# Optimization experiments

Measured on AMD Instinct MI355X. Metric: run time of the kernel, lower is better.

The kernel has to match this reference:

```python
import jax, jax.numpy as jnp
import numpy as np

N_NODES = 100000


def gcn_conv(x, W, b, src, dst, n):
    """PyG GCNConv: add self-loops, symmetric degree norm, linear, scatter-add."""
    loop = jnp.arange(n, dtype=src.dtype)
    s = jnp.concatenate([src, loop])  # source nodes (message origin)
    d = jnp.concatenate([dst, loop])  # target nodes (aggregation)
    deg = jax.ops.segment_sum(jnp.ones_like(d, dtype=x.dtype), d, num_segments=n)
    dinv = jnp.where(deg > 0, jax.lax.rsqrt(deg), 0.0)
    norm = dinv[s] * dinv[d]  # [E+N]
    h = x @ W  # [N, out]
    msg = h[s] * norm[:, None]  # [E+N, out]
    return jax.ops.segment_sum(msg, d, num_segments=n) + b


def setup_inputs() -> dict:
    key = jax.random.key(0)
    ks = jax.random.split(key, 8)
    n, e, din, dh, dout = N_NODES, 3200000, 128, 64, 6
    x = jax.random.normal(ks[0], (n, din), dtype=jnp.float32)
    edge_index = jax.random.randint(ks[1], (2, e), 0, n, dtype=jnp.int64)
    sc = lambda f: 1.0 / np.sqrt(f)
    W1 = jax.random.normal(ks[2], (din, dh), dtype=jnp.float32) * sc(din)
    b1 = jnp.zeros((dh,), dtype=jnp.float32)
    W2 = jax.random.normal(ks[3], (dh, dh), dtype=jnp.float32) * sc(dh)
    b2 = jnp.zeros((dh,), dtype=jnp.float32)
    W3 = jax.random.normal(ks[4], (dh, dout), dtype=jnp.float32) * sc(dh)
    b3 = jnp.zeros((dout,), dtype=jnp.float32)
    return {"x": x, "edge_index": edge_index, "W1": W1, "b1": b1,
            "W2": W2, "b2": b2, "W3": W3, "b3": b3}


def reference(x, edge_index, W1, b1, W2, b2, W3, b3):
    n = x.shape[0]
    src, dst = edge_index[0], edge_index[1]
    # eval mode: dropout is identity
    h = jax.nn.relu(gcn_conv(x, W1, b1, src, dst, n))
    h = jax.nn.relu(gcn_conv(h, W2, b2, src, dst, n))
    h = gcn_conv(h, W3, b3, src, dst, n)
    return jax.nn.log_softmax(h, axis=1)
```

## Files before the change

kernel.cpp:

```cpp
#include <hip/hip_runtime.h>
#include <hip/hip_fp16.h>
#include <math.h>


#define WS_ALIGN(x) (((x) + 255) & ~(size_t)255)
#define BKN 128
#define CAP 4608
#define EPT 8
#define BIN_THR 512
#define BIN_CHUNK (BIN_THR * EPT)

typedef _Float16 half8 __attribute__((ext_vector_type(8)));
typedef float floatx4 __attribute__((ext_vector_type(4)));

__global__ __launch_bounds__(BIN_THR) void bin_kernel(
    const int* __restrict__ src, const int* __restrict__ dst,
    int* __restrict__ cur, int* __restrict__ slab, int E, int NB) {
    __shared__ int counts[784];
    const int tid = threadIdx.x;
    const int base = blockIdx.x * BIN_CHUNK + tid * EPT;
    for (int i = tid; i < NB; i += BIN_THR) counts[i] = 0;
    __syncthreads();
    int b[EPT], w[EPT], lpos[EPT];
    #pragma unroll
    for (int k = 0; k < EPT; ++k) {
        int e = base + k;
        if (e < E) {
            int s = src[e], d = dst[e];
            b[k] = d >> 7;
            w[k] = (s << 7) | (d & 127);
        } else b[k] = -1;
    }
    #pragma unroll
    for (int k = 0; k < EPT; ++k)
        if (b[k] >= 0) lpos[k] = atomicAdd(&counts[b[k]], 1);
    __syncthreads();
    for (int i = tid; i < NB; i += BIN_THR) {
        int c = counts[i];
        counts[i] = c ? atomicAdd(&cur[i], c) : 0;
    }
    __syncthreads();
    #pragma unroll
    for (int k = 0; k < EPT; ++k) {
        if (b[k] >= 0) {
            int pos = counts[b[k]] + lpos[k];
            if (pos < CAP) slab[(size_t)b[k] * CAP + pos] = w[k];
        }
    }
}

__global__ __launch_bounds__(512) void bucket_sort_kernel(
    const int* __restrict__ slab, const int* __restrict__ cur,
    int* __restrict__ srcS, int2* __restrict__ rows,
    float* __restrict__ dinv, int n) {
    __shared__ int cnt[BKN], s[BKN], cursor[BKN];
    const int b = blockIdx.x, tid = threadIdx.x;
    const int m = min(cur[b], CAP);
    const int* sp = slab + (size_t)b * CAP;
    if (tid < BKN) cnt[tid] = 0;
    __syncthreads();
    for (int j = tid; j < m; j += 512) atomicAdd(&cnt[sp[j] & (BKN - 1)], 1);
    __syncthreads();
    if (tid < BKN) s[tid] = cnt[tid];
    __syncthreads();
    for (int off = 1; off < BKN; off <<= 1) {
        int v = 0;
        if (tid < BKN && tid >= off) v = s[tid - off];
        __syncthreads();
        if (tid < BKN) s[tid] += v;
        __syncthreads();
    }
    if (tid < BKN) {
        int ofs = s[tid] - cnt[tid];
        cursor[tid] = ofs;
        int node = b * BKN + tid;
        if (node < n) {
            rows[node] = make_int2(b * CAP + ofs, b * CAP + ofs + cnt[tid]);
            dinv[node] = rsqrtf((float)(cnt[tid] + 1));
        }
    }
    __syncthreads();
    for (int j = tid; j < m; j += 512) {
        int w = sp[j];
        int p = atomicAdd(&cursor[w & (BKN - 1)], 1);
        srcS[(size_t)b * CAP + p] = w >> 7;
    }
}

template <int K>
__global__ __launch_bounds__(256) void linear_mfma_f32_kernel(
    const float* __restrict__ Xf, const float* __restrict__ W,
    const float* __restrict__ dinv, _Float16* __restrict__ Y, int n) {
    constexpr int KC = K / 32;
    __shared__ _Float16 Bf[KC * 4 * 64 * 8];
    const int tid = threadIdx.x;
    for (int i = tid; i < KC * 4 * 64 * 8; i += 256) {
        int j = i & 7, lane = (i >> 3) & 63, tile = (i >> 9) & 3, kc = i >> 11;
        int k = kc * 32 + ((lane >> 4) << 3) + j;
        int col = tile * 16 + (lane & 15);
        Bf[i] = (_Float16)W[k * 64 + col];
    }
    __syncthreads();
    const int lane = tid & 63, wid = tid >> 6;
    const int mrow = lane & 15, quad = lane >> 4;
    #pragma unroll
    for (int tt = 0; tt < 4; ++tt) {
        const int base = (blockIdx.x * 4 + tt) * 64 + wid * 16;
        if (base >= n) continue;
        const int anode = min(base + mrow, n - 1);
        floatx4 acc[4] = {{0, 0, 0, 0}, {0, 0, 0, 0}, {0, 0, 0, 0}, {0, 0, 0, 0}};
        #pragma unroll
        for (int kc = 0; kc < KC; ++kc) {
            float4 xa = *(const float4*)&Xf[(size_t)anode * K + kc * 32 + quad * 8];
            float4 xb = *(const float4*)&Xf[(size_t)anode * K + kc * 32 + quad * 8 + 4];
            half8 a;
            a[0] = (_Float16)xa.x; a[1] = (_Float16)xa.y; a[2] = (_Float16)xa.z; a[3] = (_Float16)xa.w;
            a[4] = (_Float16)xb.x; a[5] = (_Float16)xb.y; a[6] = (_Float16)xb.z; a[7] = (_Float16)xb.w;
            #pragma unroll
            for (int t = 0; t < 4; ++t) {
                half8 b = *(const half8*)&Bf[((kc * 4 + t) * 64 + lane) * 8];
                acc[t] = __builtin_amdgcn_mfma_f32_16x16x32_f16(a, b, acc[t], 0, 0, 0);
            }
        }
        #pragma unroll
        for (int r = 0; r < 4; ++r) {
            int node = base + quad * 4 + r;
            if (node < n) {
                float di = dinv[node];
                #pragma unroll
                for (int t = 0; t < 4; ++t)
                    Y[(size_t)node * 64 + t * 16 + mrow] = (_Float16)(acc[t][r] * di);
            }
        }
    }
}

__global__ __launch_bounds__(256) void linear_mfma_f16_kernel(
    const _Float16* __restrict__ Xh, const float* __restrict__ W,
    const float* __restrict__ dinv, _Float16* __restrict__ Y, int n) {
    constexpr int K = 64, KC = 2;
    __shared__ _Float16 Bf[KC * 4 * 64 * 8];
    const int tid = threadIdx.x;
    for (int i = tid; i < KC * 4 * 64 * 8; i += 256) {
        int j = i & 7, lane = (i >> 3) & 63, tile = (i >> 9) & 3, kc = i >> 11;
        int k = kc * 32 + ((lane >> 4) << 3) + j;
        int col = tile * 16 + (lane & 15);
        Bf[i] = (_Float16)W[k * 64 + col];
    }
    __syncthreads();
    const int lane = tid & 63, wid = tid >> 6;
    const int mrow = lane & 15, quad = lane >> 4;
    #pragma unroll
    for (int tt = 0; tt < 4; ++tt) {
        const int base = (blockIdx.x * 4 + tt) * 64 + wid * 16;
        if (base >= n) continue;
        const int anode = min(base + mrow, n - 1);
        floatx4 acc[4] = {{0, 0, 0, 0}, {0, 0, 0, 0}, {0, 0, 0, 0}, {0, 0, 0, 0}};
        #pragma unroll
        for (int kc = 0; kc < KC; ++kc) {
            half8 a = *(const half8*)&Xh[(size_t)anode * K + kc * 32 + quad * 8];
            #pragma unroll
            for (int t = 0; t < 4; ++t) {
                half8 b = *(const half8*)&Bf[((kc * 4 + t) * 64 + lane) * 8];
                acc[t] = __builtin_amdgcn_mfma_f32_16x16x32_f16(a, b, acc[t], 0, 0, 0);
            }
        }
        #pragma unroll
        for (int r = 0; r < 4; ++r) {
            int node = base + quad * 4 + r;
            if (node < n) {
                float di = dinv[node];
                #pragma unroll
                for (int t = 0; t < 4; ++t)
                    Y[(size_t)node * 64 + t * 16 + mrow] = (_Float16)(acc[t][r] * di);
            }
        }
    }
}

__global__ __launch_bounds__(256) void linear3_kernel(const __half* __restrict__ Xh,
                                                      const float* __restrict__ W,
                                                      const float* __restrict__ dinv,
                                                      __half* __restrict__ Y, int n) {
    __shared__ float Wl[64 * 6];
    __shared__ float Xs[32][65];
    const int tid = threadIdx.x;
    for (int i = tid; i < 64 * 6; i += 256) Wl[i] = W[i];
    const int sub = tid >> 3;
    const int feat = tid & 7;
    for (int base = blockIdx.x * 32; base < n; base += gridDim.x * 32) {
        __syncthreads();
        for (int i = tid; i < 32 * 64; i += 256) {
            int r = i >> 6, c = i & 63;
            int node = base + r;
            Xs[r][c] = (node < n) ? __half2float(Xh[(size_t)node * 64 + c]) : 0.f;
        }
        __syncthreads();
        int node = base + sub;
        if (node < n) {
            float r = 0.f;
            if (feat < 6) {
                float acc = 0.f;
                #pragma unroll
                for (int k = 0; k < 64; ++k) acc = fmaf(Xs[sub][k], Wl[k * 6 + feat], acc);
                r = acc * dinv[node];
            }
            Y[(size_t)node * 8 + feat] = __float2half_rn(r);
        }
    }
}

__global__ __launch_bounds__(256) void agg64_kernel(
    const _Float16* __restrict__ Hs, const float* __restrict__ dinv,
    const int* __restrict__ srcS, const int2* __restrict__ rows,
    const float* __restrict__ bias, _Float16* __restrict__ Out,
    int n, int do_relu) {
    const int wave = (blockIdx.x * blockDim.x + threadIdx.x) >> 6;
    const int lane = threadIdx.x & 63;
    if (wave >= n) return;
    const int slot = lane >> 3;
    const int f8 = lane & 7;
    const int2 row = rows[wave];
    const int beg = row.x, end = row.y;
    half8 hA, hB;
    #pragma unroll
    for (int i = 0; i < 8; ++i) { hA[i] = (_Float16)0.f; hB[i] = (_Float16)0.f; }
    int j = beg;
    for (; j + 32 <= end; j += 32) {
        int s0 = srcS[j      + slot];
        int s1 = srcS[j + 8  + slot];
        int s2 = srcS[j + 16 + slot];
        int s3 = srcS[j + 24 + slot];
        half8 v0 = *(const half8*)&Hs[(size_t)s0 * 64 + f8 * 8];
        half8 v1 = *(const half8*)&Hs[(size_t)s1 * 64 + f8 * 8];
        half8 v2 = *(const half8*)&Hs[(size_t)s2 * 64 + f8 * 8];
        half8 v3 = *(const half8*)&Hs[(size_t)s3 * 64 + f8 * 8];
        hA += v0; hB += v1; hA += v2; hB += v3;
    }
    for (; j + 16 <= end; j += 16) {
        int s0 = srcS[j + slot];
        int s1 = srcS[j + 8 + slot];
        half8 v0 = *(const half8*)&Hs[(size_t)s0 * 64 + f8 * 8];
        half8 v1 = *(const half8*)&Hs[(size_t)s1 * 64 + f8 * 8];
        hA += v0; hB += v1;
    }
    for (; j < end; j += 8) {
        int jj = j + slot;
        if (jj < end) {
            half8 v = *(const half8*)&Hs[(size_t)srcS[jj] * 64 + f8 * 8];
            hA += v;
        }
    }
    half8 ht = hA + hB;
    #pragma unroll
    for (int mask = 8; mask <= 32; mask <<= 1) {
        int4 ci = *(int4*)&ht, oi;
        oi.x = __shfl_xor(ci.x, mask);
        oi.y = __shfl_xor(ci.y, mask);
        oi.z = __shfl_xor(ci.z, mask);
        oi.w = __shfl_xor(ci.w, mask);
        ht += *(half8*)&oi;
    }
    half8 self = *(const half8*)&Hs[(size_t)wave * 64 + f8 * 8];
    const float di = dinv[wave];
    float4 b0 = *(const float4*)&bias[f8 * 8];
    float4 b1 = *(const float4*)&bias[f8 * 8 + 4];
    float bb[8] = {b0.x, b0.y, b0.z, b0.w, b1.x, b1.y, b1.z, b1.w};
    half8 o;
    #pragma unroll
    for (int i = 0; i < 8; ++i) {
        float t = ((float)ht[i] + (float)self[i]) * di + bb[i];
        if (do_relu) t = fmaxf(t, 0.f);
        o[i] = (_Float16)t;
    }
    if (slot == 0) *(half8*)&Out[(size_t)wave * 64 + f8 * 8] = o;
}

__global__ __launch_bounds__(256) void agg6_lsm_kernel(
    const _Float16* __restrict__ Hs6, const float* __restrict__ dinv,
    const int* __restrict__ srcS, const int2* __restrict__ rows,
    const float* __restrict__ bias, float* __restrict__ out, int n) {
    const int wave = (blockIdx.x * blockDim.x + threadIdx.x) >> 6;
    const int lane = threadIdx.x & 63;
    if (wave >= n) return;
    const int2 row = rows[wave];
    const int beg = row.x, end = row.y;
    half8 ht;
    #pragma unroll
    for (int i = 0; i < 8; ++i) ht[i] = (_Float16)0.f;
    for (int j = beg + lane; j < end; j += 64) {
        int s = srcS[j];
        ht += *(const half8*)&Hs6[(size_t)s * 8];
    }
    #pragma unroll
    for (int mask = 1; mask <= 32; mask <<= 1) {
        int4 ci = *(int4*)&ht, oi;
        oi.x = __shfl_xor(ci.x, mask);
        oi.y = __shfl_xor(ci.y, mask);
        oi.z = __shfl_xor(ci.z, mask);
        oi.w = __shfl_xor(ci.w, mask);
        ht += *(half8*)&oi;
    }
    half8 self = *(const half8*)&Hs6[(size_t)wave * 8];
    const float di = dinv[wave];
    float a[6];
    #pragma unroll
    for (int q = 0; q < 6; ++q)
        a[q] = ((float)ht[q] + (float)self[q]) * di + bias[q];
    float mx = a[0];
    #pragma unroll
    for (int q = 1; q < 6; ++q) mx = fmaxf(mx, a[q]);
    float sum = 0.f;
    #pragma unroll
    for (int q = 0; q < 6; ++q) sum += expf(a[q] - mx);
    float lse = mx + logf(sum);
    if (lane == 0) {
        float* op = &out[(size_t)wave * 6];
        *(float2*)(op)     = make_float2(a[0] - lse, a[1] - lse);
        *(float2*)(op + 2) = make_float2(a[2] - lse, a[3] - lse);
        *(float2*)(op + 4) = make_float2(a[4] - lse, a[5] - lse);
    }
}

extern "C" void kernel_launch(void* const* d_in, const int* in_sizes, int n_in,
                              void* d_out, int out_size, void* d_ws, size_t ws_size,
                              hipStream_t stream) {
    const float* x  = (const float*)d_in[0];
    const int*   ei = (const int*)d_in[1];
    const float* W1 = (const float*)d_in[2];
    const float* b1 = (const float*)d_in[3];
    const float* W2 = (const float*)d_in[4];
    const float* b2 = (const float*)d_in[5];
    const float* W3 = (const float*)d_in[6];
    const float* b3 = (const float*)d_in[7];
    float* out = (float*)d_out;

    const int n = in_sizes[0] / 128;
    const int E = in_sizes[1] / 2;
    const int* src = ei;
    const int* dst = ei + E;
    const int NB = (n + BKN - 1) / BKN;

    char* ws = (char*)d_ws;
    auto carve = [&](size_t bytes) { char* p = ws; ws += WS_ALIGN(bytes); return p; };
    int*      cur  = (int*)     carve((size_t)NB * 4);
    float*    dinv = (float*)   carve((size_t)n * 4);
    int*      slab = (int*)     carve((size_t)NB * CAP * 4);
    int*      srcS = (int*)     carve((size_t)NB * CAP * 4);
    int2*     rows = (int2*)    carve((size_t)n * 8);
    _Float16* hsA  = (_Float16*)carve((size_t)n * 64 * 2 + 4096);
    _Float16* hsB  = (_Float16*)carve((size_t)n * 64 * 2 + 4096);
    _Float16* hsC  = (_Float16*)carve((size_t)n * 8 * 2);
    (void)ws_size; (void)n_in; (void)out_size;

    hipMemsetAsync(cur, 0, (size_t)NB * 4, stream);
    bin_kernel<<<(E + BIN_CHUNK - 1) / BIN_CHUNK, BIN_THR, 0, stream>>>(src, dst, cur, slab, E, NB);
    bucket_sort_kernel<<<NB, 512, 0, stream>>>(slab, cur, srcS, rows, dinv, n);

    const int aggGrid = (n + 3) / 4;
    const int linGrid = (n + 255) / 256;

    linear_mfma_f32_kernel<128><<<linGrid, 256, 0, stream>>>(x, W1, dinv, hsA, n);
    agg64_kernel<<<aggGrid, 256, 0, stream>>>(hsA, dinv, srcS, rows, b1, hsB, n, 1);

    linear_mfma_f16_kernel<<<linGrid, 256, 0, stream>>>(hsB, W2, dinv, hsA, n);
    agg64_kernel<<<aggGrid, 256, 0, stream>>>(hsA, dinv, srcS, rows, b2, hsB, n, 1);

    linear3_kernel<<<2048, 256, 0, stream>>>((const __half*)hsB, W3, dinv, (__half*)hsC, n);
    agg6_lsm_kernel<<<aggGrid, 256, 0, stream>>>(hsC, dinv, srcS, rows, b3, out, n);
}
```

Measured before the change: 355.9 us.

## Store hidden features in 16-column chunks and aggregate per chunk

Hidden activations now use a chunked column layout, four planes of [n][16] fp16 instead of [n][64]. The 64-wide aggregation kernel runs one pass per chunk, with four nodes per wave, so each gathered plane (about 3.2 MB) is more likely to stay resident in cache during the random gather. Index loads and output stores use nontemporal hints so they do not evict the feature plane. In exchange, srcS and rows are read four times per layer, and the linear kernels load and store with strided chunk addressing.

```diff
diff --git a/kernel.cpp b/kernel.cpp
--- a/kernel.cpp
+++ b/kernel.cpp
@@ -12,6 +12,7 @@
 
 typedef _Float16 half8 __attribute__((ext_vector_type(8)));
 typedef float floatx4 __attribute__((ext_vector_type(4)));
+typedef int intx4 __attribute__((ext_vector_type(4)));
 
 __global__ __launch_bounds__(BIN_THR) void bin_kernel(
     const int* __restrict__ src, const int* __restrict__ dst,
@@ -129,7 +130,7 @@
                 float di = dinv[node];
                 #pragma unroll
                 for (int t = 0; t < 4; ++t)
-                    Y[(size_t)node * 64 + t * 16 + mrow] = (_Float16)(acc[t][r] * di);
+                    Y[((size_t)t * n + node) * 16 + mrow] = (_Float16)(acc[t][r] * di);
             }
         }
     }
@@ -138,7 +139,7 @@
 __global__ __launch_bounds__(256) void linear_mfma_f16_kernel(
     const _Float16* __restrict__ Xh, const float* __restrict__ W,
     const float* __restrict__ dinv, _Float16* __restrict__ Y, int n) {
-    constexpr int K = 64, KC = 2;
+    constexpr int KC = 2;
     __shared__ _Float16 Bf[KC * 4 * 64 * 8];
     const int tid = threadIdx.x;
     for (int i = tid; i < KC * 4 * 64 * 8; i += 256) {
@@ -158,7 +159,7 @@
         floatx4 acc[4] = {{0, 0, 0, 0}, {0, 0, 0, 0}, {0, 0, 0, 0}, {0, 0, 0, 0}};
         #pragma unroll
         for (int kc = 0; kc < KC; ++kc) {
-            half8 a = *(const half8*)&Xh[(size_t)anode * K + kc * 32 + quad * 8];
+            half8 a = *(const half8*)&Xh[((size_t)(2 * kc + (quad >> 1)) * n + anode) * 16 + (quad & 1) * 8];
             #pragma unroll
             for (int t = 0; t < 4; ++t) {
                 half8 b = *(const half8*)&Bf[((kc * 4 + t) * 64 + lane) * 8];
@@ -172,13 +173,13 @@
                 float di = dinv[node];
                 #pragma unroll
                 for (int t = 0; t < 4; ++t)
-                    Y[(size_t)node * 64 + t * 16 + mrow] = (_Float16)(acc[t][r] * di);
-            }
-        }
-    }
-}
-
-__global__ __launch_bounds__(256) void linear3_kernel(const __half* __restrict__ Xh,
+                    Y[((size_t)t * n + node) * 16 + mrow] = (_Float16)(acc[t][r] * di);
+            }
+        }
+    }
+}
+
+__global__ __launch_bounds__(256) void linear3_kernel(const _Float16* __restrict__ Xh,
                                                       const float* __restrict__ W,
                                                       const float* __restrict__ dinv,
                                                       __half* __restrict__ Y, int n) {
@@ -188,12 +189,19 @@
     for (int i = tid; i < 64 * 6; i += 256) Wl[i] = W[i];
     const int sub = tid >> 3;
     const int feat = tid & 7;
+    const int sr = tid >> 3, c8 = tid & 7;
     for (int base = blockIdx.x * 32; base < n; base += gridDim.x * 32) {
         __syncthreads();
-        for (int i = tid; i < 32 * 64; i += 256) {
-            int r = i >> 6, c = i & 63;
-            int node = base + r;
-            Xs[r][c] = (node < n) ? __half2float(Xh[(size_t)node * 64 + c]) : 0.f;
+        {
+            int node = base + sr;
+            half8 v;
+            if (node < n)
+                v = *(const half8*)&Xh[((size_t)(c8 >> 1) * n + node) * 16 + (c8 & 1) * 8];
+            else
+                #pragma unroll
+                for (int k = 0; k < 8; ++k) v[k] = (_Float16)0.f;
+            #pragma unroll
+            for (int k = 0; k < 8; ++k) Xs[sr][c8 * 8 + k] = (float)v[k];
         }
         __syncthreads();
         int node = base + sub;
@@ -210,50 +218,38 @@
     }
 }
 
-__global__ __launch_bounds__(256) void agg64_kernel(
-    const _Float16* __restrict__ Hs, const float* __restrict__ dinv,
+__global__ __launch_bounds__(256) void agg64c_kernel(
+    const _Float16* __restrict__ Hc, const float* __restrict__ dinv,
     const int* __restrict__ srcS, const int2* __restrict__ rows,
     const float* __restrict__ bias, _Float16* __restrict__ Out,
-    int n, int do_relu) {
-    const int wave = (blockIdx.x * blockDim.x + threadIdx.x) >> 6;
+    int n, int nwgpc, int do_relu) {
+    const int chunk = blockIdx.x / nwgpc;
     const int lane = threadIdx.x & 63;
-    if (wave >= n) return;
-    const int slot = lane >> 3;
-    const int f8 = lane & 7;
-    const int2 row = rows[wave];
-    const int beg = row.x, end = row.y;
+    const int node = ((blockIdx.x % nwgpc) * 4 + (threadIdx.x >> 6)) * 4 + (lane >> 4);
+    if (node >= n) return;
+    const int slot = (lane >> 1) & 7;
+    const int h = lane & 1;
+    const char* Hb = (const char*)(Hc + (size_t)chunk * n * 16);
+    const int2 row = rows[node];
+    const int end = row.y;
     half8 hA, hB;
     #pragma unroll
     for (int i = 0; i < 8; ++i) { hA[i] = (_Float16)0.f; hB[i] = (_Float16)0.f; }
-    int j = beg;
-    for (; j + 32 <= end; j += 32) {
-        int s0 = srcS[j      + slot];
-        int s1 = srcS[j + 8  + slot];
-        int s2 = srcS[j + 16 + slot];
-        int s3 = srcS[j + 24 + slot];
-        half8 v0 = *(const half8*)&Hs[(size_t)s0 * 64 + f8 * 8];
-        half8 v1 = *(const half8*)&Hs[(size_t)s1 * 64 + f8 * 8];
-        half8 v2 = *(const half8*)&Hs[(size_t)s2 * 64 + f8 * 8];
-        half8 v3 = *(const half8*)&Hs[(size_t)s3 * 64 + f8 * 8];
-        hA += v0; hB += v1; hA += v2; hB += v3;
-    }
-    for (; j + 16 <= end; j += 16) {
-        int s0 = srcS[j + slot];
-        int s1 = srcS[j + 8 + slot];
-        half8 v0 = *(const half8*)&Hs[(size_t)s0 * 64 + f8 * 8];
-        half8 v1 = *(const half8*)&Hs[(size_t)s1 * 64 + f8 * 8];
+    int jj = row.x + slot;
+    for (; jj + 8 < end; jj += 16) {
+        int s0 = __builtin_nontemporal_load(srcS + jj);
+        int s1 = __builtin_nontemporal_load(srcS + jj + 8);
+        half8 v0 = *(const half8*)(Hb + (s0 << 5) + (h << 4));
+        half8 v1 = *(const half8*)(Hb + (s1 << 5) + (h << 4));
         hA += v0; hB += v1;
     }
-    for (; j < end; j += 8) {
-        int jj = j + slot;
-        if (jj < end) {
-            half8 v = *(const half8*)&Hs[(size_t)srcS[jj] * 64 + f8 * 8];
-            hA += v;
-        }
+    if (jj < end) {
+        int s0 = __builtin_nontemporal_load(srcS + jj);
+        hA += *(const half8*)(Hb + (s0 << 5) + (h << 4));
     }
     half8 ht = hA + hB;
     #pragma unroll
-    for (int mask = 8; mask <= 32; mask <<= 1) {
+    for (int mask = 2; mask <= 8; mask <<= 1) {
         int4 ci = *(int4*)&ht, oi;
         oi.x = __shfl_xor(ci.x, mask);
         oi.y = __shfl_xor(ci.y, mask);
@@ -261,19 +257,20 @@
         oi.w = __shfl_xor(ci.w, mask);
         ht += *(half8*)&oi;
     }
-    half8 self = *(const half8*)&Hs[(size_t)wave * 64 + f8 * 8];
-    const float di = dinv[wave];
-    float4 b0 = *(const float4*)&bias[f8 * 8];
-    float4 b1 = *(const float4*)&bias[f8 * 8 + 4];
-    float bb[8] = {b0.x, b0.y, b0.z, b0.w, b1.x, b1.y, b1.z, b1.w};
+    half8 self = *(const half8*)(Hb + (node << 5) + (h << 4));
+    const float di = dinv[node];
+    const float* bp = bias + chunk * 16 + h * 8;
     half8 o;
     #pragma unroll
     for (int i = 0; i < 8; ++i) {
-        float t = ((float)ht[i] + (float)self[i]) * di + bb[i];
+        float t = ((float)ht[i] + (float)self[i]) * di + bp[i];
         if (do_relu) t = fmaxf(t, 0.f);
         o[i] = (_Float16)t;
     }
-    if (slot == 0) *(half8*)&Out[(size_t)wave * 64 + f8 * 8] = o;
+    if ((lane & 14) == 0) {
+        intx4* op = (intx4*)((char*)Out + (size_t)chunk * n * 32 + (node << 5) + (h << 4));
+        __builtin_nontemporal_store(*(intx4*)&o, op);
+    }
 }
 
 __global__ __launch_bounds__(256) void agg6_lsm_kernel(
@@ -289,7 +286,7 @@
     #pragma unroll
     for (int i = 0; i < 8; ++i) ht[i] = (_Float16)0.f;
     for (int j = beg + lane; j < end; j += 64) {
-        int s = srcS[j];
+        int s = __builtin_nontemporal_load(srcS + j);
         ht += *(const half8*)&Hs6[(size_t)s * 8];
     }
     #pragma unroll
@@ -353,19 +350,19 @@
     _Float16* hsC  = (_Float16*)carve((size_t)n * 8 * 2);
     (void)ws_size; (void)n_in; (void)out_size;
 
-    hipMemsetAsync(cur, 0, (size_t)NB * 4, stream);
+    (void)hipMemsetAsync(cur, 0, (size_t)NB * 4, stream);
     bin_kernel<<<(E + BIN_CHUNK - 1) / BIN_CHUNK, BIN_THR, 0, stream>>>(src, dst, cur, slab, E, NB);
     bucket_sort_kernel<<<NB, 512, 0, stream>>>(slab, cur, srcS, rows, dinv, n);
 
-    const int aggGrid = (n + 3) / 4;
+    const int nwgpc = (n + 15) / 16;
     const int linGrid = (n + 255) / 256;
 
     linear_mfma_f32_kernel<128><<<linGrid, 256, 0, stream>>>(x, W1, dinv, hsA, n);
-    agg64_kernel<<<aggGrid, 256, 0, stream>>>(hsA, dinv, srcS, rows, b1, hsB, n, 1);
+    agg64c_kernel<<<nwgpc * 4, 256, 0, stream>>>(hsA, dinv, srcS, rows, b1, hsB, n, nwgpc, 1);
 
     linear_mfma_f16_kernel<<<linGrid, 256, 0, stream>>>(hsB, W2, dinv, hsA, n);
-    agg64_kernel<<<aggGrid, 256, 0, stream>>>(hsA, dinv, srcS, rows, b2, hsB, n, 1);
-
-    linear3_kernel<<<2048, 256, 0, stream>>>((const __half*)hsB, W3, dinv, (__half*)hsC, n);
-    agg6_lsm_kernel<<<aggGrid, 256, 0, stream>>>(hsC, dinv, srcS, rows, b3, out, n);
-}
+    agg64c_kernel<<<nwgpc * 4, 256, 0, stream>>>(hsA, dinv, srcS, rows, b2, hsB, n, nwgpc, 1);
+
+    linear3_kernel<<<2048, 256, 0, stream>>>(hsB, W3, dinv, (__half*)hsC, n);
+    agg6_lsm_kernel<<<(n + 3) / 4, 256, 0, stream>>>(hsC, dinv, srcS, rows, b3, out, n);
+}
```

Measured after the change: 447.8 us. 25.8% more time.

## Stage binned edges in shared memory and double bucket width for coalesced slab writes

Applied to the files above, without the earlier changes.

Destination buckets now cover 256 nodes instead of 128, which halves the number of buckets and doubles the slab capacity per bucket. The binning kernel scans per-block bucket counts, stages edges in shared memory sorted by bucket, and then writes contiguous runs to the global slab. Each output index recovers its bucket with a binary search over the scan. This replaces per-thread scattered global writes with grouped runs. The cost is extra shared-memory traffic, more barriers and the search work per element, and the later bucket sort uses only half of its threads on 256-wide buckets.

```diff
diff --git a/kernel.cpp b/kernel.cpp
--- a/kernel.cpp
+++ b/kernel.cpp
@@ -4,8 +4,8 @@
 
 
 #define WS_ALIGN(x) (((x) + 255) & ~(size_t)255)
-#define BKN 128
-#define CAP 4608
+#define BKN 256
+#define CAP 9216
 #define EPT 8
 #define BIN_THR 512
 #define BIN_CHUNK (BIN_THR * EPT)
@@ -16,36 +16,53 @@
 __global__ __launch_bounds__(BIN_THR) void bin_kernel(
     const int* __restrict__ src, const int* __restrict__ dst,
     int* __restrict__ cur, int* __restrict__ slab, int E, int NB) {
-    __shared__ int counts[784];
+    __shared__ int cnt[512];
+    __shared__ int incl[512];
+    __shared__ int gbase[512];
+    __shared__ int stag[BIN_CHUNK];
     const int tid = threadIdx.x;
     const int base = blockIdx.x * BIN_CHUNK + tid * EPT;
-    for (int i = tid; i < NB; i += BIN_THR) counts[i] = 0;
-    __syncthreads();
-    int b[EPT], w[EPT], lpos[EPT];
+    cnt[tid] = 0;
+    __syncthreads();
+    int b[EPT], w[EPT], lp[EPT];
     #pragma unroll
     for (int k = 0; k < EPT; ++k) {
         int e = base + k;
         if (e < E) {
             int s = src[e], d = dst[e];
-            b[k] = d >> 7;
-            w[k] = (s << 7) | (d & 127);
+            b[k] = d >> 8;
+            w[k] = (s << 8) | (d & 255);
         } else b[k] = -1;
     }
     #pragma unroll
     for (int k = 0; k < EPT; ++k)
-        if (b[k] >= 0) lpos[k] = atomicAdd(&counts[b[k]], 1);
-    __syncthreads();
-    for (int i = tid; i < NB; i += BIN_THR) {
-        int c = counts[i];
-        counts[i] = c ? atomicAdd(&cur[i], c) : 0;
-    }
-    __syncthreads();
-    #pragma unroll
-    for (int k = 0; k < EPT; ++k) {
-        if (b[k] >= 0) {
-            int pos = counts[b[k]] + lpos[k];
-            if (pos < CAP) slab[(size_t)b[k] * CAP + pos] = w[k];
-        }
+        if (b[k] >= 0) lp[k] = atomicAdd(&cnt[b[k]], 1);
+    __syncthreads();
+    incl[tid] = cnt[tid];
+    __syncthreads();
+    for (int off = 1; off < 512; off <<= 1) {
+        int v = 0;
+        if (tid >= off) v = incl[tid - off];
+        __syncthreads();
+        incl[tid] += v;
+        __syncthreads();
+    }
+    if (tid < NB) {
+        int c = cnt[tid];
+        gbase[tid] = c ? atomicAdd(&cur[tid], c) : 0;
+    }
+    #pragma unroll
+    for (int k = 0; k < EPT; ++k)
+        if (b[k] >= 0) stag[incl[b[k]] - cnt[b[k]] + lp[k]] = w[k];
+    __syncthreads();
+    const int total = incl[NB - 1];
+    for (int idx = tid; idx < total; idx += BIN_THR) {
+        int wv = stag[idx];
+        int lo = 0, hi = NB - 1;
+        while (lo < hi) { int mid = (lo + hi) >> 1; if (incl[mid] > idx) hi = mid; else lo = mid + 1; }
+        int excl = incl[lo] - cnt[lo];
+        int p = gbase[lo] + (idx - excl);
+        if (p < CAP) slab[(size_t)lo * CAP + p] = wv;
     }
 }
 
@@ -83,7 +100,7 @@
     for (int j = tid; j < m; j += 512) {
         int w = sp[j];
         int p = atomicAdd(&cursor[w & (BKN - 1)], 1);
-        srcS[(size_t)b * CAP + p] = w >> 7;
+        srcS[(size_t)b * CAP + p] = w >> 8;
     }
 }
 
@@ -353,7 +370,7 @@
     _Float16* hsC  = (_Float16*)carve((size_t)n * 8 * 2);
     (void)ws_size; (void)n_in; (void)out_size;
 
-    hipMemsetAsync(cur, 0, (size_t)NB * 4, stream);
+    (void)hipMemsetAsync(cur, 0, (size_t)NB * 4, stream);
     bin_kernel<<<(E + BIN_CHUNK - 1) / BIN_CHUNK, BIN_THR, 0, stream>>>(src, dst, cur, slab, E, NB);
     bucket_sort_kernel<<<NB, 512, 0, stream>>>(slab, cur, srcS, rows, dinv, n);
 
@@ -367,5 +384,5 @@
     agg64_kernel<<<aggGrid, 256, 0, stream>>>(hsA, dinv, srcS, rows, b2, hsB, n, 1);
 
     linear3_kernel<<<2048, 256, 0, stream>>>((const __half*)hsB, W3, dinv, (__half*)hsC, n);
-    agg6_lsm_kernel<<<aggGrid, 256, 0, stream>>>(hsC, dinv, srcS, rows, b3, out, n);
-}
+    agg6_lsm_kernel<<<(n + 3) / 4, 256, 0, stream>>>(hsC, dinv, srcS, rows, b3, out, n);
+}
```

After: 356.0 us. About the same (+0.0%).

## Replace bucketed slab sort with global count/prefix-sum/scatter CSR build

Applied to the files above, without the earlier changes.

Replaces the two-pass bucket binning (shared-memory bins into a fixed-capacity slab, then a per-bucket sort) with a plain CSR build: global atomic degree count, a per-block prefix sum that recomputes the block base by summing all earlier degrees, and an atomic-cursor scatter of source ids. This removes the CAP overflow truncation and the slab buffer, but relies on global atomics over random destinations and a prefix kernel whose per-block base reduction grows with block index. It also halves the rows handled per block in the linear kernels, doubling their grid.

```diff
diff --git a/kernel.cpp b/kernel.cpp
--- a/kernel.cpp
+++ b/kernel.cpp
@@ -4,86 +4,72 @@
 
 
 #define WS_ALIGN(x) (((x) + 255) & ~(size_t)255)
-#define BKN 128
-#define CAP 4608
 #define EPT 8
-#define BIN_THR 512
-#define BIN_CHUNK (BIN_THR * EPT)
+#define CNT_THR 512
+#define CNT_CHUNK (CNT_THR * EPT)
 
 typedef _Float16 half8 __attribute__((ext_vector_type(8)));
 typedef float floatx4 __attribute__((ext_vector_type(4)));
 
-__global__ __launch_bounds__(BIN_THR) void bin_kernel(
+__global__ __launch_bounds__(CNT_THR) void count_kernel(
+    const int* __restrict__ dst, int* __restrict__ deg, int E) {
+    const int base = blockIdx.x * CNT_CHUNK + threadIdx.x * EPT;
+    #pragma unroll
+    for (int k = 0; k < EPT; ++k) {
+        int e = base + k;
+        if (e < E) atomicAdd(&deg[dst[e]], 1);
+    }
+}
+
+__global__ __launch_bounds__(256) void rows_kernel(
+    const int* __restrict__ deg, int2* __restrict__ rows,
+    int* __restrict__ cursor, float* __restrict__ dinv, int n) {
+    __shared__ int red[256];
+    __shared__ int sc[256];
+    const int tid = threadIdx.x;
+    const int limit = blockIdx.x * 256;
+    int psum = 0;
+    for (int i = tid * 4; i < limit; i += 256 * 4) {
+        const int4 v = *(const int4*)&deg[i];
+        psum += v.x + v.y + v.z + v.w;
+    }
+    red[tid] = psum;
+    __syncthreads();
+    for (int off = 128; off > 0; off >>= 1) {
+        if (tid < off) red[tid] += red[tid + off];
+        __syncthreads();
+    }
+    const int base = red[0];
+    const int node = limit + tid;
+    const int d = (node < n) ? deg[node] : 0;
+    sc[tid] = d;
+    __syncthreads();
+    for (int off = 1; off < 256; off <<= 1) {
+        int v = (tid >= off) ? sc[tid - off] : 0;
+        __syncthreads();
+        sc[tid] += v;
+        __syncthreads();
+    }
+    if (node < n) {
+        const int start = base + sc[tid] - d;
+        rows[node] = make_int2(start, start + d);
+        cursor[node] = start;
+        dinv[node] = rsqrtf((float)(d + 1));
+    }
+}
+
+__global__ __launch_bounds__(CNT_THR) void scatter_kernel(
     const int* __restrict__ src, const int* __restrict__ dst,
-    int* __restrict__ cur, int* __restrict__ slab, int E, int NB) {
-    __shared__ int counts[784];
-    const int tid = threadIdx.x;
-    const int base = blockIdx.x * BIN_CHUNK + tid * EPT;
-    for (int i = tid; i < NB; i += BIN_THR) counts[i] = 0;
-    __syncthreads();
-    int b[EPT], w[EPT], lpos[EPT];
+    int* __restrict__ cursor, int* __restrict__ srcS, int E) {
+    const int base = blockIdx.x * CNT_CHUNK + threadIdx.x * EPT;
     #pragma unroll
     for (int k = 0; k < EPT; ++k) {
         int e = base + k;
         if (e < E) {
             int s = src[e], d = dst[e];
-            b[k] = d >> 7;
-            w[k] = (s << 7) | (d & 127);
-        } else b[k] = -1;
-    }
-    #pragma unroll
-    for (int k = 0; k < EPT; ++k)
-        if (b[k] >= 0) lpos[k] = atomicAdd(&counts[b[k]], 1);
-    __syncthreads();
-    for (int i = tid; i < NB; i += BIN_THR) {
-        int c = counts[i];
-        counts[i] = c ? atomicAdd(&cur[i], c) : 0;
-    }
-    __syncthreads();
-    #pragma unroll
-    for (int k = 0; k < EPT; ++k) {
-        if (b[k] >= 0) {
-            int pos = counts[b[k]] + lpos[k];
-            if (pos < CAP) slab[(size_t)b[k] * CAP + pos] = w[k];
-        }
-    }
-}
-
-__global__ __launch_bounds__(512) void bucket_sort_kernel(
-    const int* __restrict__ slab, const int* __restrict__ cur,
-    int* __restrict__ srcS, int2* __restrict__ rows,
-    float* __restrict__ dinv, int n) {
-    __shared__ int cnt[BKN], s[BKN], cursor[BKN];
-    const int b = blockIdx.x, tid = threadIdx.x;
-    const int m = min(cur[b], CAP);
-    const int* sp = slab + (size_t)b * CAP;
-    if (tid < BKN) cnt[tid] = 0;
-    __syncthreads();
-    for (int j = tid; j < m; j += 512) atomicAdd(&cnt[sp[j] & (BKN - 1)], 1);
-    __syncthreads();
-    if (tid < BKN) s[tid] = cnt[tid];
-    __syncthreads();
-    for (int off = 1; off < BKN; off <<= 1) {
-        int v = 0;
-        if (tid < BKN && tid >= off) v = s[tid - off];
-        __syncthreads();
-        if (tid < BKN) s[tid] += v;
-        __syncthreads();
-    }
-    if (tid < BKN) {
-        int ofs = s[tid] - cnt[tid];
-        cursor[tid] = ofs;
-        int node = b * BKN + tid;
-        if (node < n) {
-            rows[node] = make_int2(b * CAP + ofs, b * CAP + ofs + cnt[tid]);
-            dinv[node] = rsqrtf((float)(cnt[tid] + 1));
-        }
-    }
-    __syncthreads();
-    for (int j = tid; j < m; j += 512) {
-        int w = sp[j];
-        int p = atomicAdd(&cursor[w & (BKN - 1)], 1);
-        srcS[(size_t)b * CAP + p] = w >> 7;
+            int p = atomicAdd(&cursor[d], 1);
+            srcS[p] = s;
+        }
     }
 }
 
@@ -104,8 +90,8 @@
     const int lane = tid & 63, wid = tid >> 6;
     const int mrow = lane & 15, quad = lane >> 4;
     #pragma unroll
-    for (int tt = 0; tt < 4; ++tt) {
-        const int base = (blockIdx.x * 4 + tt) * 64 + wid * 16;
+    for (int tt = 0; tt < 2; ++tt) {
+        const int base = (blockIdx.x * 2 + tt) * 64 + wid * 16;
         if (base >= n) continue;
         const int anode = min(base + mrow, n - 1);
         floatx4 acc[4] = {{0, 0, 0, 0}, {0, 0, 0, 0}, {0, 0, 0, 0}, {0, 0, 0, 0}};
@@ -151,8 +137,8 @@
     const int lane = tid & 63, wid = tid >> 6;
     const int mrow = lane & 15, quad = lane >> 4;
     #pragma unroll
-    for (int tt = 0; tt < 4; ++tt) {
-        const int base = (blockIdx.x * 4 + tt) * 64 + wid * 16;
+    for (int tt = 0; tt < 2; ++tt) {
+        const int base = (blockIdx.x * 2 + tt) * 64 + wid * 16;
         if (base >= n) continue;
         const int anode = min(base + mrow, n - 1);
         floatx4 acc[4] = {{0, 0, 0, 0}, {0, 0, 0, 0}, {0, 0, 0, 0}, {0, 0, 0, 0}};
@@ -339,26 +325,27 @@
     const int E = in_sizes[1] / 2;
     const int* src = ei;
     const int* dst = ei + E;
-    const int NB = (n + BKN - 1) / BKN;
 
     char* ws = (char*)d_ws;
     auto carve = [&](size_t bytes) { char* p = ws; ws += WS_ALIGN(bytes); return p; };
-    int*      cur  = (int*)     carve((size_t)NB * 4);
-    float*    dinv = (float*)   carve((size_t)n * 4);
-    int*      slab = (int*)     carve((size_t)NB * CAP * 4);
-    int*      srcS = (int*)     carve((size_t)NB * CAP * 4);
-    int2*     rows = (int2*)    carve((size_t)n * 8);
-    _Float16* hsA  = (_Float16*)carve((size_t)n * 64 * 2 + 4096);
-    _Float16* hsB  = (_Float16*)carve((size_t)n * 64 * 2 + 4096);
-    _Float16* hsC  = (_Float16*)carve((size_t)n * 8 * 2);
+    int*      deg    = (int*)     carve((size_t)n * 4);
+    int*      cursor = (int*)     carve((size_t)n * 4);
+    float*    dinv   = (float*)   carve((size_t)n * 4);
+    int2*     rows   = (int2*)    carve((size_t)n * 8);
+    int*      srcS   = (int*)     carve((size_t)E * 4);
+    _Float16* hsA    = (_Float16*)carve((size_t)n * 64 * 2 + 4096);
+    _Float16* hsB    = (_Float16*)carve((size_t)n * 64 * 2 + 4096);
+    _Float16* hsC    = (_Float16*)carve((size_t)n * 8 * 2);
     (void)ws_size; (void)n_in; (void)out_size;
 
-    hipMemsetAsync(cur, 0, (size_t)NB * 4, stream);
-    bin_kernel<<<(E + BIN_CHUNK - 1) / BIN_CHUNK, BIN_THR, 0, stream>>>(src, dst, cur, slab, E, NB);
-    bucket_sort_kernel<<<NB, 512, 0, stream>>>(slab, cur, srcS, rows, dinv, n);
+    (void)hipMemsetAsync(deg, 0, (size_t)n * 4, stream);
+    const int edgeGrid = (E + CNT_CHUNK - 1) / CNT_CHUNK;
+    count_kernel<<<edgeGrid, CNT_THR, 0, stream>>>(dst, deg, E);
+    rows_kernel<<<(n + 255) / 256, 256, 0, stream>>>(deg, rows, cursor, dinv, n);
+    scatter_kernel<<<edgeGrid, CNT_THR, 0, stream>>>(src, dst, cursor, srcS, E);
 
     const int aggGrid = (n + 3) / 4;
-    const int linGrid = (n + 255) / 256;
+    const int linGrid = (n + 127) / 128;
 
     linear_mfma_f32_kernel<128><<<linGrid, 256, 0, stream>>>(x, W1, dinv, hsA, n);
     agg64_kernel<<<aggGrid, 256, 0, stream>>>(hsA, dinv, srcS, rows, b1, hsB, n, 1);
```

Result: slower. 617.8 us (+73.6%).
